# Kernel tuning notes

Measured on AMD Instinct MI355X. Metric: run time of the kernel, lower is better.

The kernel has to match this reference:

```python
import jax, jax.numpy as jnp
import numpy as np

MAX_NUM_ATOMS = 13  # hard-coded in the module; num_params = 13**2 = 169


def setup_inputs() -> dict:
    key = jax.random.key(0)
    k1, k2, k3, k4, k5 = jax.random.split(key, 5)
    M, N, ORDER, H, O = 200, 1024, 3, 512, 512
    x = jax.random.randint(k1, (M, 3), 0, MAX_NUM_ATOMS, dtype=jnp.int64 if jax.config.jax_enable_x64 else jnp.int32)
    fact = jax.random.randint(k2, (N, 2), 0, M, dtype=jnp.int64 if jax.config.jax_enable_x64 else jnp.int32)
    inp = jax.random.normal(k3, (ORDER, N, H), dtype=jnp.float32)
    params = jax.random.normal(k4, (MAX_NUM_ATOMS ** 2, H, O), dtype=jnp.float32) * 0.05
    bias = jax.random.normal(k5, (MAX_NUM_ATOMS ** 2, 1, O), dtype=jnp.float32) * 0.05
    return {"x": x, "fact": fact, "inp": inp, "params": params, "bias": bias,
            "msg_to": 0, "order": 3}


def reference(x, fact, inp, params, bias, msg_to, order):
    # elementwise product of all inp[i] with i != msg_to  -> [N, H]
    keep = jnp.array([i for i in range(order) if i != msg_to])
    fact_prod = jnp.prod(inp[keep], axis=0)
    # per-row weight-matrix id from atom pair  -> [N]
    atom_pairs = x[fact[:, 0]][:, 1:]              # [N, 2]
    ids = atom_pairs[:, 0] * MAX_NUM_ATOMS + atom_pairs[:, 1]
    W = params[ids]                                # [N, H, O] gathered table
    b = bias[ids][:, 0, :]                         # [N, O]
    return jnp.einsum('nh,nho->no', fact_prod, W) + b
```

## Files before the change

kernel.cpp:

```cpp
#include <hip/hip_runtime.h>

#define NATOMS 13
#define NP (NATOMS * NATOMS)

constexpr int N_ = 1024;
constexpr int H_ = 512;
constexpr int O_ = 512;
constexpr int RB = 4;
constexpr int OSPLIT = 2;
constexpr int OC = O_ / OSPLIT;
constexpr int MAXQUAD = 384;
constexpr int NB = MAXQUAD * OSPLIT;
constexpr int RECS = 8;

__global__ void build_quads(const int* __restrict__ x,
                            const int* __restrict__ fact,
                            int* __restrict__ ws, int N) {
    __shared__ int s_id[N_];
    __shared__ int s_cnt[NP];
    __shared__ int s_start[NP];
    __shared__ int s_qstart[NP];
    __shared__ int s_pos[NP];
    __shared__ int s_sorted[N_];
    const int tid = threadIdx.x, bd = blockDim.x;

    for (int i = tid; i < NP; i += bd) { s_cnt[i] = 0; s_pos[i] = 0; }
    __syncthreads();
    for (int n = tid; n < N; n += bd) {
        const int f0 = fact[2 * n];
        const int id = x[f0 * 3 + 1] * NATOMS + x[f0 * 3 + 2];
        s_id[n] = id;
        atomicAdd(&s_cnt[id], 1);
    }
    __syncthreads();
    if (tid == 0) {
        int run = 0, qrun = 0;
        for (int g = 0; g < NP; ++g) {
            s_start[g] = run;   run  += s_cnt[g];
            s_qstart[g] = qrun; qrun += (s_cnt[g] + RB - 1) / RB;
        }
        ws[0] = qrun;
    }
    __syncthreads();
    for (int n = tid; n < N; n += bd) {
        const int id = s_id[n];
        const int p = atomicAdd(&s_pos[id], 1);
        s_sorted[s_start[id] + p] = n;
    }
    __syncthreads();
    for (int g = tid; g < NP; g += bd) {
        const int c = s_cnt[g], st = s_start[g], qs = s_qstart[g];
        const int nq = (c + RB - 1) / RB;
        for (int k = 0; k < nq; ++k) {
            int* rec = ws + 16 + (size_t)(qs + k) * RECS;
            for (int r = 0; r < RB; ++r) {
                const int idx = k * RB + r;
                rec[r] = (idx < c) ? s_sorted[st + idx] : -1;
            }
            rec[RB] = g;
        }
    }
}

__global__ __launch_bounds__(256)
void quad_gemv(const int* __restrict__ ws,
               const float* __restrict__ inp,
               const float* __restrict__ params,
               const float* __restrict__ bias,
               const int* __restrict__ msg_to_p,
               const int* __restrict__ order_p,
               float* __restrict__ out, int N) {
    constexpr int q = NB / 8;
    const int b = blockIdx.x;
    const int Lg = (b & 7) * q + (b >> 3);
    const int quad = Lg >> 1;
    const int op   = Lg & 1;

    if (quad >= ws[0]) return;
    const int* rec = ws + 16 + (size_t)quad * RECS;
    const int id = rec[RB];

    const int msg_to = *msg_to_p;
    const int order  = *order_p;
    const int tid = threadIdx.x;
    const int sub = tid >> 6;
    const int l   = tid & 63;
    const int o0  = op * OC;

    __shared__ float  fp_s[H_][RB];
    __shared__ float4 red[4][RB][64];

#pragma unroll
    for (int r = 0; r < RB; ++r) {
        const int row = rec[r];
        if (row >= 0) {
#pragma unroll
            for (int k = 0; k < H_ / 256; ++k) {
                const int h = k * 256 + tid;
                float p = 1.0f;
                for (int i = 0; i < order; ++i)
                    if (i != msg_to)
                        p *= inp[((size_t)i * N + row) * H_ + h];
                fp_s[h][r] = p;
            }
        } else {
#pragma unroll
            for (int k = 0; k < H_ / 256; ++k) fp_s[k * 256 + tid][r] = 0.0f;
        }
    }
    __syncthreads();

    const float* __restrict__ wbase =
        params + (size_t)id * H_ * O_ + (size_t)sub * O_ + o0 + 4 * l;

    float4 a0 = make_float4(0,0,0,0), a1 = a0, a2 = a0, a3 = a0;

#define FMA4(acc, s, wv) acc.x += (s) * wv.x; acc.y += (s) * wv.y;    \
                         acc.z += (s) * wv.z; acc.w += (s) * wv.w;
#pragma unroll 8
    for (int hh = 0; hh < H_ / 4; ++hh) {
        const float4 w = *(const float4*)(wbase + (size_t)hh * 4 * O_);
        const float4 f = *(const float4*)&fp_s[4 * hh + sub][0];
        FMA4(a0, f.x, w)
        FMA4(a1, f.y, w)
        FMA4(a2, f.z, w)
        FMA4(a3, f.w, w)
    }
#undef FMA4

    red[sub][0][l] = a0;
    red[sub][1][l] = a1;
    red[sub][2][l] = a2;
    red[sub][3][l] = a3;
    __syncthreads();

    const int row = rec[sub];
    if (row >= 0) {
        const float4 p0 = red[0][sub][l];
        const float4 p1 = red[1][sub][l];
        const float4 p2 = red[2][sub][l];
        const float4 p3 = red[3][sub][l];
        const float4 bv = *(const float4*)(bias + (size_t)id * O_ + o0 + 4 * l);
        float4 s;
        s.x = p0.x + p1.x + p2.x + p3.x + bv.x;
        s.y = p0.y + p1.y + p2.y + p3.y + bv.y;
        s.z = p0.z + p1.z + p2.z + p3.z + bv.z;
        s.w = p0.w + p1.w + p2.w + p3.w + bv.w;
        *(float4*)(out + (size_t)row * O_ + o0 + 4 * l) = s;
    }
}

extern "C" void kernel_launch(void* const* d_in, const int* in_sizes, int n_in,
                              void* d_out, int out_size, void* d_ws, size_t ws_size,
                              hipStream_t stream) {
    const int*   x      = (const int*)d_in[0];
    const int*   fact   = (const int*)d_in[1];
    const float* inp    = (const float*)d_in[2];
    const float* params = (const float*)d_in[3];
    const float* bias   = (const float*)d_in[4];
    const int*   msg_to = (const int*)d_in[5];
    const int*   order  = (const int*)d_in[6];
    float*       out    = (float*)d_out;

    const int N = in_sizes[1] / 2;
    int* ws = (int*)d_ws;

    hipLaunchKernelGGL(build_quads, dim3(1), dim3(256), 0, stream,
                       x, fact, ws, N);

    hipLaunchKernelGGL(quad_gemv, dim3(NB), dim3(256), 0, stream,
                       ws, inp, params, bias, msg_to, order, out, N);
}
```

Before: 51.52 us.

## Fuse quad-building into GEMV kernel, recomputing grouping per block in shared memory

Removes the separate single-block build_quads launch and its workspace round-trip. Every GEMV block now recomputes the atom-pair ids, histogram and prefix sums itself, plus a stable deterministic sort done by one thread per group, all in shared memory aliased onto the reduction buffer. Each block then binary-searches its group from its quad index. This removes a serial launch and dependency but repeats the gather and sort work redundantly in all 768 blocks, and the per-group serial scan over 1024 ids adds latency before the GEMV starts.

```diff
diff --git a/kernel.cpp b/kernel.cpp
--- a/kernel.cpp
+++ b/kernel.cpp
@@ -11,22 +11,37 @@
 constexpr int OC = O_ / OSPLIT;
 constexpr int MAXQUAD = 384;
 constexpr int NB = MAXQUAD * OSPLIT;
-constexpr int RECS = 8;
 
-__global__ void build_quads(const int* __restrict__ x,
-                            const int* __restrict__ fact,
-                            int* __restrict__ ws, int N) {
-    __shared__ int s_id[N_];
-    __shared__ int s_cnt[NP];
-    __shared__ int s_start[NP];
-    __shared__ int s_qstart[NP];
-    __shared__ int s_pos[NP];
-    __shared__ int s_sorted[N_];
-    const int tid = threadIdx.x, bd = blockDim.x;
+__global__ __launch_bounds__(256)
+void fused_gemv(const int* __restrict__ x,
+                const int* __restrict__ fact,
+                const float* __restrict__ inp,
+                const float* __restrict__ params,
+                const float* __restrict__ bias,
+                const int* __restrict__ msg_to_p,
+                const int* __restrict__ order_p,
+                float* __restrict__ out, int N) {
+    constexpr int q8 = NB / 8;
+    const int b = blockIdx.x;
+    const int Lg = (b & 7) * q8 + (b >> 3);
+    const int quad = Lg >> 1;
+    const int op   = Lg & 1;
 
-    for (int i = tid; i < NP; i += bd) { s_cnt[i] = 0; s_pos[i] = 0; }
+    const int tid = threadIdx.x;
+
+    __shared__ float  fp_s[H_][RB];
+    __shared__ float4 red[4][RB][64];
+    int* s_id     = (int*)&red[0][0][0];
+    int* s_sorted = s_id + N_;
+    int* s_cnt    = s_sorted + N_;
+    int* s_start  = s_cnt + NP;
+    int* s_qstart = s_start + NP;
+
+    for (int i = tid; i < NP; i += 256) s_cnt[i] = 0;
     __syncthreads();
-    for (int n = tid; n < N; n += bd) {
+#pragma unroll
+    for (int k = 0; k < N_ / 256; ++k) {
+        const int n = k * 256 + tid;
         const int f0 = fact[2 * n];
         const int id = x[f0 * 3 + 1] * NATOMS + x[f0 * 3 + 2];
         s_id[n] = id;
@@ -37,62 +52,50 @@
         int run = 0, qrun = 0;
         for (int g = 0; g < NP; ++g) {
             s_start[g] = run;   run  += s_cnt[g];
-            s_qstart[g] = qrun; qrun += (s_cnt[g] + RB - 1) / RB;
+            s_qstart[g] = qrun; qrun += (s_cnt[g] + RB - 1) >> 2;
         }
-        ws[0] = qrun;
+        s_qstart[NP] = qrun;
     }
     __syncthreads();
-    for (int n = tid; n < N; n += bd) {
-        const int id = s_id[n];
-        const int p = atomicAdd(&s_pos[id], 1);
-        s_sorted[s_start[id] + p] = n;
+    if (tid < NP) {
+        const int g = tid;
+        int c = 0;
+        const int st = s_start[g];
+        for (int n4 = 0; n4 < N_ / 4; ++n4) {
+            const int4 v = ((const int4*)s_id)[n4];
+            if (v.x == g) s_sorted[st + c++] = 4 * n4 + 0;
+            if (v.y == g) s_sorted[st + c++] = 4 * n4 + 1;
+            if (v.z == g) s_sorted[st + c++] = 4 * n4 + 2;
+            if (v.w == g) s_sorted[st + c++] = 4 * n4 + 3;
+        }
     }
     __syncthreads();
-    for (int g = tid; g < NP; g += bd) {
-        const int c = s_cnt[g], st = s_start[g], qs = s_qstart[g];
-        const int nq = (c + RB - 1) / RB;
-        for (int k = 0; k < nq; ++k) {
-            int* rec = ws + 16 + (size_t)(qs + k) * RECS;
-            for (int r = 0; r < RB; ++r) {
-                const int idx = k * RB + r;
-                rec[r] = (idx < c) ? s_sorted[st + idx] : -1;
-            }
-            rec[RB] = g;
-        }
+
+    if (quad >= s_qstart[NP]) return;
+
+    int glo = 0, ghi = NP;
+    while (ghi - glo > 1) {
+        const int gm = (glo + ghi) >> 1;
+        if (s_qstart[gm] <= quad) glo = gm; else ghi = gm;
     }
-}
-
-__global__ __launch_bounds__(256)
-void quad_gemv(const int* __restrict__ ws,
-               const float* __restrict__ inp,
-               const float* __restrict__ params,
-               const float* __restrict__ bias,
-               const int* __restrict__ msg_to_p,
-               const int* __restrict__ order_p,
-               float* __restrict__ out, int N) {
-    constexpr int q = NB / 8;
-    const int b = blockIdx.x;
-    const int Lg = (b & 7) * q + (b >> 3);
-    const int quad = Lg >> 1;
-    const int op   = Lg & 1;
-
-    if (quad >= ws[0]) return;
-    const int* rec = ws + 16 + (size_t)quad * RECS;
-    const int id = rec[RB];
+    const int id = glo;
+    const int kq = quad - s_qstart[id];
+    const int c  = s_cnt[id];
+    const int st = s_start[id];
 
     const int msg_to = *msg_to_p;
     const int order  = *order_p;
-    const int tid = threadIdx.x;
     const int sub = tid >> 6;
     const int l   = tid & 63;
     const int o0  = op * OC;
 
-    __shared__ float  fp_s[H_][RB];
-    __shared__ float4 red[4][RB][64];
+    const int sidx  = RB * kq + sub;
+    const int myrow = (sidx < c) ? s_sorted[st + sidx] : -1;
 
 #pragma unroll
     for (int r = 0; r < RB; ++r) {
-        const int row = rec[r];
+        const int idx = RB * kq + r;
+        const int row = (idx < c) ? s_sorted[st + idx] : -1;
         if (row >= 0) {
 #pragma unroll
             for (int k = 0; k < H_ / 256; ++k) {
@@ -128,14 +131,14 @@
     }
 #undef FMA4
 
+    __syncthreads();
     red[sub][0][l] = a0;
     red[sub][1][l] = a1;
     red[sub][2][l] = a2;
     red[sub][3][l] = a3;
     __syncthreads();
 
-    const int row = rec[sub];
-    if (row >= 0) {
+    if (myrow >= 0) {
         const float4 p0 = red[0][sub][l];
         const float4 p1 = red[1][sub][l];
         const float4 p2 = red[2][sub][l];
@@ -146,7 +149,7 @@
         s.y = p0.y + p1.y + p2.y + p3.y + bv.y;
         s.z = p0.z + p1.z + p2.z + p3.z + bv.z;
         s.w = p0.w + p1.w + p2.w + p3.w + bv.w;
-        *(float4*)(out + (size_t)row * O_ + o0 + 4 * l) = s;
+        *(float4*)(out + (size_t)myrow * O_ + o0 + 4 * l) = s;
     }
 }
 
@@ -163,11 +166,7 @@
     float*       out    = (float*)d_out;
 
     const int N = in_sizes[1] / 2;
-    int* ws = (int*)d_ws;
 
-    hipLaunchKernelGGL(build_quads, dim3(1), dim3(256), 0, stream,
-                       x, fact, ws, N);
-
-    hipLaunchKernelGGL(quad_gemv, dim3(NB), dim3(256), 0, stream,
-                       ws, inp, params, bias, msg_to, order, out, N);
+    hipLaunchKernelGGL(fused_gemv, dim3(NB), dim3(256), 0, stream,
+                       x, fact, inp, params, bias, msg_to, order, out, N);
 }
```

After: 86.10 us. +67.1%, slower.
